# Performance work log

Measured on AMD Instinct MI355X. Metric: run time of the kernel, lower is better.

The kernel has to match this reference:

```python
import jax, jax.numpy as jnp
import numpy as np

B, D, H, E, K = 8192, 1024, 256, 16, 4


def setup_inputs() -> dict:
    key = jax.random.key(0)
    ks = jax.random.split(key, 6)
    s_d = D ** -0.5
    s_h = H ** -0.5
    return {
        "x": jax.random.normal(ks[0], (B, D), dtype=jnp.float32),
        "route_w": jax.random.normal(ks[1], (E, D), dtype=jnp.float32) * s_d,
        "w1": jax.random.normal(ks[2], (E, H, D), dtype=jnp.float32) * s_d,
        "b1": jax.random.normal(ks[3], (E, H), dtype=jnp.float32) * s_d,
        "w2": jax.random.normal(ks[4], (E, D, H), dtype=jnp.float32) * s_h,
        "b2": jax.random.normal(ks[5], (E, D), dtype=jnp.float32) * s_h,
    }


def _moe_forward(x, route_w, w1, b1, w2, b2):
    # Router: logits (B, E) -> top-k softmax weights scattered back to (B, E).
    logits = x @ route_w.T
    top_vals, top_idx = jax.lax.top_k(logits, K)
    top_w = jax.nn.softmax(top_vals, axis=-1)
    rows = jnp.arange(x.shape[0])[:, None]
    weights = jnp.zeros_like(logits).at[rows, top_idx].set(top_w)  # (B, E)

    # Experts: out = sum_e w[:, e] * relu(relu(x W1e^T + b1e) W2e^T + b2e)
    # Non-selected experts have weight 0, so dense-then-weight matches the
    # original masked gather/scatter math exactly (dropout = 0).
    def step(out, params_e):
        W1, bb1, W2, bb2, we = params_e
        h = jax.nn.relu(x @ W1.T + bb1)       # (B, H)
        y = jax.nn.relu(h @ W2.T + bb2)       # (B, D)
        return out + y * we[:, None], None

    out0 = jnp.zeros_like(x)
    out, _ = jax.lax.scan(step, out0, (w1, b1, w2, b2, weights.T))
    return out


def reference(x, route_w, w1, b1, w2, b2):
    return _moe_forward(x, route_w, w1, b1, w2, b2)
```

## Files before the change

### kernel.cpp

```cpp
#include <hip/hip_runtime.h>
#include <stdint.h>

typedef unsigned short u16;
typedef __attribute__((ext_vector_type(8))) short bf16x8;
typedef __attribute__((ext_vector_type(4))) float f32x4;
typedef __attribute__((ext_vector_type(8))) u16 u16x8;
typedef __attribute__((ext_vector_type(4))) u16 u16x4;

#define NTOK 8192
#define DDIM 1024
#define HDIM 256
#define NEXP 16
#define MAXT 272
#define MAXMT (MAXT * 2)
#define MAXSLOT (MAXT * 128)

__device__ __forceinline__ u16 f2bf(float f) {
  uint32_t u = __builtin_bit_cast(uint32_t, f);
  u += 0x7FFFu + ((u >> 16) & 1u);
  return (u16)(u >> 16);
}
__device__ __forceinline__ float bf2f(u16 h) {
  return __builtin_bit_cast(float, (uint32_t)h << 16);
}

__device__ __forceinline__ void gll16(const void* g, void* l) {
  __builtin_amdgcn_global_load_lds((const __attribute__((address_space(1))) void*)g,
                                   (__attribute__((address_space(3))) void*)l,
                                   16, 0, 0);
}

__global__ __launch_bounds__(256) void cvt_kernel(const float* __restrict__ in,
                                                  u16* __restrict__ out) {
  size_t i = ((size_t)blockIdx.x * 256 + threadIdx.x) * 8;
  const float4 a = *(const float4*)(in + i);
  const float4 b = *(const float4*)(in + i + 4);
  u16x8 o;
  o[0] = f2bf(a.x); o[1] = f2bf(a.y); o[2] = f2bf(a.z); o[3] = f2bf(a.w);
  o[4] = f2bf(b.x); o[5] = f2bf(b.y); o[6] = f2bf(b.z); o[7] = f2bf(b.w);
  *(u16x8*)(out + i) = o;
}

__global__ __launch_bounds__(256) void zero_out_kernel(float* __restrict__ p) {
  size_t i = ((size_t)blockIdx.x * 256 + threadIdx.x) * 4;
  *(float4*)(p + i) = (float4){0.f, 0.f, 0.f, 0.f};
}

__global__ __launch_bounds__(256) void router_kernel(const float* __restrict__ x,
                                                     const float* __restrict__ rw,
                                                     int* __restrict__ epack,
                                                     float* __restrict__ ew,
                                                     u16* __restrict__ xbf) {
  __shared__ __align__(16) uint8_t rwlds[65536];
  const int tid = threadIdx.x;

#pragma unroll
  for (int i = 0; i < 16; ++i) {
    int byte = (i * 256 + tid) * 16;
    int sw = byte ^ (((byte >> 8) & 7) << 4);
    *(float4*)(rwlds + sw) = *(const float4*)((const uint8_t*)rw + byte);
  }
  __syncthreads();

  const int lane = tid & 63, wid = tid >> 6;
  const int s = lane & 15;
  const int tok = blockIdx.x * 16 + wid * 4 + (lane >> 4);
  const float* xrow = x + (size_t)tok * DDIM;
  u16* xbrow = xbf + (size_t)tok * DDIM;

  double acc[NEXP];
#pragma unroll
  for (int e = 0; e < NEXP; ++e) acc[e] = 0.0;

#pragma unroll 4
  for (int g = 0; g < 16; ++g) {
    const int d = s * 64 + g * 4;
    float4 xv = *(const float4*)(xrow + d);
    u16x4 o;
    o[0] = f2bf(xv.x); o[1] = f2bf(xv.y); o[2] = f2bf(xv.z); o[3] = f2bf(xv.w);
    *(u16x4*)(xbrow + d) = o;
    const double x0 = xv.x, x1 = xv.y, x2 = xv.z, x3 = xv.w;
    const int roff = (s * 256 + g * 16) ^ ((s & 7) << 4);
#pragma unroll
    for (int e = 0; e < NEXP; ++e) {
      float4 rv = *(const float4*)(rwlds + e * 4096 + roff);
      acc[e] = fma(x0, (double)rv.x, acc[e]);
      acc[e] = fma(x1, (double)rv.y, acc[e]);
      acc[e] = fma(x2, (double)rv.z, acc[e]);
      acc[e] = fma(x3, (double)rv.w, acc[e]);
    }
  }

#define FOLD(H, M)                                                   \
  _Pragma("unroll") for (int i = 0; i < H; ++i) {                    \
    double send = (lane & M) ? acc[i] : acc[i + H];                  \
    double recv = __shfl_xor(send, M);                               \
    acc[i] = ((lane & M) ? acc[i + H] : acc[i]) + recv;              \
  }
  FOLD(8, 1)
  FOLD(4, 2)
  FOLD(2, 4)
  FOLD(1, 8)
#undef FOLD
  const int e_mine = ((lane & 1) << 3) | ((lane & 2) << 1) |
                     ((lane & 4) >> 1) | ((lane & 8) >> 3);

  double val = acc[0];
  double tv[4]; int tidx[4];
#pragma unroll
  for (int k = 0; k < 4; ++k) {
    double bv = val; int be = e_mine;
#pragma unroll
    for (int m = 1; m < 16; m <<= 1) {
      double ov = __shfl_xor(bv, m);
      int oe = __shfl_xor(be, m);
      if (ov > bv || (ov == bv && oe < be)) { bv = ov; be = oe; }
    }
    tv[k] = bv; tidx[k] = be;
    if (e_mine == be) val = -1.0e300;
  }

  if ((lane & 15) == 0) {
    float m0 = (float)tv[0];
    float w[4]; float sum = 0.f;
#pragma unroll
    for (int k = 0; k < 4; ++k) { w[k] = expf((float)tv[k] - m0); sum += w[k]; }
    epack[tok] = tidx[0] | (tidx[1] << 8) | (tidx[2] << 16) | (tidx[3] << 24);
#pragma unroll
    for (int k = 0; k < 4; ++k) ew[tok * 4 + k] = w[k] / sum;
  }
}

__global__ __launch_bounds__(1024) void compact_kernel(const int* __restrict__ epack,
                                                       const float* __restrict__ ew,
                                                       int* __restrict__ texp,
                                                       int* __restrict__ perm,
                                                       float* __restrict__ wsl,
                                                       int* __restrict__ islot) {
  __shared__ int wave_cnt[16][NEXP];
  __shared__ int counts_sm[NEXP];
  __shared__ int wtot[16], wave_off[16];
  const int e = blockIdx.x;
  const int tid = threadIdx.x, lane = tid & 63, w = tid >> 6;

  int ep[8]; unsigned m[8];
#pragma unroll
  for (int j = 0; j < 8; ++j) {
    ep[j] = epack[tid * 8 + j];
    m[j] = (1u << (ep[j] & 255)) | (1u << ((ep[j] >> 8) & 255)) |
           (1u << ((ep[j] >> 16) & 255)) | (1u << ((ep[j] >> 24) & 255));
  }
#pragma unroll
  for (int ee = 0; ee < NEXP; ++ee) {
    int c = 0;
#pragma unroll
    for (int j = 0; j < 8; ++j) c += (m[j] >> ee) & 1u;
#pragma unroll
    for (int off = 32; off > 0; off >>= 1) c += __shfl_xor(c, off);
    if (lane == 0) wave_cnt[w][ee] = c;
  }
  unsigned fm = 0;
#pragma unroll
  for (int j = 0; j < 8; ++j) fm |= ((m[j] >> e) & 1u) << j;
  int s = __popc(fm);
  int incl = s;
#pragma unroll
  for (int d = 1; d < 64; d <<= 1) {
    int t2 = __shfl_up(incl, d);
    if (lane >= d) incl += t2;
  }
  if (lane == 63) wtot[w] = incl;
  __syncthreads();
  if (tid < NEXP) {
    int c = 0;
    for (int w2 = 0; w2 < 16; ++w2) c += wave_cnt[w2][tid];
    counts_sm[tid] = c;
  }
  if (tid == 0) {
    int run = 0;
    for (int w2 = 0; w2 < 16; ++w2) { wave_off[w2] = run; run += wtot[w2]; }
  }
  __syncthreads();
  int base = 0;
  for (int ee = 0; ee < NEXP; ++ee)
    if (ee < e) base += ((counts_sm[ee] + 127) >> 7) << 7;
  int pos = base + wave_off[w] + (incl - s);
#pragma unroll
  for (int j = 0; j < 8; ++j) {
    if ((fm >> j) & 1u) {
      int tok = tid * 8 + j;
      int b0 = ep[j] & 255, b1 = (ep[j] >> 8) & 255, b2_ = (ep[j] >> 16) & 255;
      int k = (b0 == e) ? 0 : ((b1 == e) ? 1 : ((b2_ == e) ? 2 : 3));
      perm[pos] = tok;
      wsl[pos] = ew[tok * 4 + k];
      islot[tok * 4 + k] = pos;
      ++pos;
    }
  }
  int cnt = counts_sm[e];
  int pad = (((cnt + 127) >> 7) << 7) - cnt;
  if (tid < pad) { perm[base + cnt + tid] = 0; wsl[base + cnt + tid] = 0.f; }
  if (e == 0 && tid == 0) {
    int tc = 0;
    for (int ee = 0; ee < NEXP; ++ee) {
      int nt = (counts_sm[ee] + 127) >> 7;
      for (int i = 0; i < nt; ++i) texp[tc++] = ee;
    }
    for (; tc < MAXT; ++tc) texp[tc] = -1;
  }
}

__device__ __forceinline__ void stage128(const u16* __restrict__ base, int ld,
                                         int kbase, uint8_t* dst, int tid) {
#pragma unroll
  for (int i = 0; i < 4; ++i) {
    int u = i * 256 + tid;
    int row = u >> 3, g = u & 7;
    gll16(base + (size_t)row * ld + kbase + ((g ^ (row & 7)) << 3), dst + u * 16);
  }
}
__device__ __forceinline__ void stage64(const u16* __restrict__ base, int ld,
                                        int kbase, uint8_t* dst, int tid) {
#pragma unroll
  for (int i = 0; i < 2; ++i) {
    int u = i * 256 + tid;
    int row = u >> 3, g = u & 7;
    gll16(base + (size_t)row * ld + kbase + ((g ^ (row & 7)) << 3), dst + u * 16);
  }
}
__device__ __forceinline__ void stage_gather64(const u16* __restrict__ xbf,
                                               const int tok[2], int kbase,
                                               uint8_t* dst, int tid) {
#pragma unroll
  for (int i = 0; i < 2; ++i) {
    int u = i * 256 + tid;
    int g = u & 7;
    gll16(xbf + (size_t)tok[i] * DDIM + kbase + ((g ^ ((u >> 3) & 7)) << 3), dst + u * 16);
  }
}

__device__ __forceinline__ void mma64(const uint8_t* Ab, const uint8_t* Bb,
                                      f32x4 acc[2][4], int wm, int wn,
                                      int lrow, int lk) {
#pragma unroll
  for (int s = 0; s < 2; ++s) {
    bf16x8 af[2], bfr[4];
#pragma unroll
    for (int f = 0; f < 2; ++f) {
      int ar = wm * 32 + f * 16 + lrow;
      af[f] = *(const bf16x8*)(Ab + ar * 128 + ((((s << 2) | lk) ^ (ar & 7)) << 4));
    }
#pragma unroll
    for (int f = 0; f < 4; ++f) {
      int br = wn * 64 + f * 16 + lrow;
      bfr[f] = *(const bf16x8*)(Bb + br * 128 + ((((s << 2) | lk) ^ (br & 7)) << 4));
    }
#pragma unroll
    for (int i = 0; i < 2; ++i)
#pragma unroll
      for (int j = 0; j < 4; ++j)
        acc[i][j] = __builtin_amdgcn_mfma_f32_16x16x32_bf16(af[i], bfr[j], acc[i][j], 0, 0, 0);
  }
}

__global__ __launch_bounds__(256) void gemm1_kernel(const u16* __restrict__ xbf,
                                                    const u16* __restrict__ w1bf,
                                                    const float* __restrict__ b1,
                                                    const int* __restrict__ texp,
                                                    const int* __restrict__ perm,
                                                    u16* __restrict__ Hc, int mt0) {
  __shared__ __align__(16) uint8_t smem[2][24576];
  const int mt = mt0 + blockIdx.x;
  const int e = (mt < MAXMT) ? texp[mt >> 1] : -1;
  if (e < 0) return;
  const int n0 = blockIdx.y * 128;
  const int tid = threadIdx.x;
  const int lane = tid & 63, wid = tid >> 6;
  const int wm = wid >> 1, wn = wid & 1;
  const int lrow = lane & 15, lk = lane >> 4;

  int tok[2];
#pragma unroll
  for (int i = 0; i < 2; ++i) tok[i] = perm[mt * 64 + ((i * 256 + tid) >> 3)];
  const u16* Bsrc = w1bf + ((size_t)e * HDIM + n0) * DDIM;

  f32x4 acc[2][4];
#pragma unroll
  for (int i = 0; i < 2; ++i)
#pragma unroll
    for (int j = 0; j < 4; ++j) acc[i][j] = (f32x4){0.f, 0.f, 0.f, 0.f};

  stage_gather64(xbf, tok, 0, smem[0], tid);
  stage128(Bsrc, DDIM, 0, smem[0] + 8192, tid);
  __syncthreads();
  int cur = 0;
  for (int kt = 0; kt < 16; ++kt) {
    if (kt < 15) {
      stage_gather64(xbf, tok, (kt + 1) * 64, smem[cur ^ 1], tid);
      stage128(Bsrc, DDIM, (kt + 1) * 64, smem[cur ^ 1] + 8192, tid);
    }
    mma64(smem[cur], smem[cur] + 8192, acc, wm, wn, lrow, lk);
    __syncthreads();
    cur ^= 1;
  }
#pragma unroll
  for (int j = 0; j < 4; ++j) {
    int n = n0 + wn * 64 + j * 16 + lrow;
    float bias = b1[e * HDIM + n];
#pragma unroll
    for (int i = 0; i < 2; ++i) {
      int rloc = (mt - mt0) * 64 + wm * 32 + i * 16 + lk * 4;
#pragma unroll
      for (int r = 0; r < 4; ++r) {
        float h = fmaxf(acc[i][j][r] + bias, 0.f);
        Hc[((size_t)rloc + r) * HDIM + n] = f2bf(h);
      }
    }
  }
}

__global__ __launch_bounds__(256) void gemm2_main_kernel(const u16* __restrict__ Hc,
                                                         const u16* __restrict__ w2bf,
                                                         const float* __restrict__ b2,
                                                         const int* __restrict__ texp,
                                                         u16* __restrict__ ybuf,
                                                         int nbase, int NC) {
  __shared__ __align__(16) uint8_t smem[2][24576];
  const int mt = blockIdx.x;
  const int e = texp[mt >> 1];
  if (e < 0) return;
  const int nl0 = blockIdx.y * 128;
  const int tid = threadIdx.x;
  const int lane = tid & 63, wid = tid >> 6;
  const int wm = wid >> 1, wn = wid & 1;
  const int lrow = lane & 15, lk = lane >> 4;

  const u16* Asrc = Hc + (size_t)mt * 64 * HDIM;
  const u16* Bsrc = w2bf + ((size_t)e * DDIM + nbase + nl0) * HDIM;

  f32x4 acc[2][4];
#pragma unroll
  for (int i = 0; i < 2; ++i)
#pragma unroll
    for (int j = 0; j < 4; ++j) acc[i][j] = (f32x4){0.f, 0.f, 0.f, 0.f};

  stage64(Asrc, HDIM, 0, smem[0], tid);
  stage128(Bsrc, HDIM, 0, smem[0] + 8192, tid);
  __syncthreads();
  int cur = 0;
  for (int kt = 0; kt < 4; ++kt) {
    if (kt < 3) {
      stage64(Asrc, HDIM, (kt + 1) * 64, smem[cur ^ 1], tid);
      stage128(Bsrc, HDIM, (kt + 1) * 64, smem[cur ^ 1] + 8192, tid);
    }
    mma64(smem[cur], smem[cur] + 8192, acc, wm, wn, lrow, lk);
    __syncthreads();
    cur ^= 1;
  }
  float bias[4];
#pragma unroll
  for (int j = 0; j < 4; ++j)
    bias[j] = b2[e * DDIM + nbase + nl0 + wn * 64 + j * 16 + lrow];
#pragma unroll
  for (int i = 0; i < 2; ++i) {
#pragma unroll
    for (int r = 0; r < 4; ++r) {
      int slot = mt * 64 + wm * 32 + i * 16 + lk * 4 + r;
#pragma unroll
      for (int j = 0; j < 4; ++j) {
        int nloc = nl0 + wn * 64 + j * 16 + lrow;
        float h = fmaxf(acc[i][j][r] + bias[j], 0.f);
        ybuf[(size_t)slot * NC + nloc] = f2bf(h);
      }
    }
  }
}

__global__ __launch_bounds__(256) void gemm2_fb_kernel(const u16* __restrict__ Hc,
                                                       const u16* __restrict__ w2bf,
                                                       const float* __restrict__ b2,
                                                       const int* __restrict__ texp,
                                                       const int* __restrict__ perm,
                                                       const float* __restrict__ wsl,
                                                       float* __restrict__ out, int mt0) {
  __shared__ __align__(16) uint8_t smem[2][24576];
  const int mt = mt0 + blockIdx.x;
  const int e = (mt < MAXMT) ? texp[mt >> 1] : -1;
  if (e < 0) return;
  const int nl0 = blockIdx.y * 128;
  const int tid = threadIdx.x;
  const int lane = tid & 63, wid = tid >> 6;
  const int wm = wid >> 1, wn = wid & 1;
  const int lrow = lane & 15, lk = lane >> 4;

  const u16* Asrc = Hc + (size_t)(mt - mt0) * 64 * HDIM;
  const u16* Bsrc = w2bf + ((size_t)e * DDIM + nl0) * HDIM;

  f32x4 acc[2][4];
#pragma unroll
  for (int i = 0; i < 2; ++i)
#pragma unroll
    for (int j = 0; j < 4; ++j) acc[i][j] = (f32x4){0.f, 0.f, 0.f, 0.f};

  stage64(Asrc, HDIM, 0, smem[0], tid);
  stage128(Bsrc, HDIM, 0, smem[0] + 8192, tid);
  __syncthreads();
  int cur = 0;
  for (int kt = 0; kt < 4; ++kt) {
    if (kt < 3) {
      stage64(Asrc, HDIM, (kt + 1) * 64, smem[cur ^ 1], tid);
      stage128(Bsrc, HDIM, (kt + 1) * 64, smem[cur ^ 1] + 8192, tid);
    }
    mma64(smem[cur], smem[cur] + 8192, acc, wm, wn, lrow, lk);
    __syncthreads();
    cur ^= 1;
  }
  float bias[4];
#pragma unroll
  for (int j = 0; j < 4; ++j)
    bias[j] = b2[e * DDIM + nl0 + wn * 64 + j * 16 + lrow];
#pragma unroll
  for (int i = 0; i < 2; ++i) {
#pragma unroll
    for (int r = 0; r < 4; ++r) {
      int slot = mt * 64 + wm * 32 + i * 16 + lk * 4 + r;
      int tokn = perm[slot];
      float w = wsl[slot];
#pragma unroll
      for (int j = 0; j < 4; ++j) {
        int n = nl0 + wn * 64 + j * 16 + lrow;
        float h = fmaxf(acc[i][j][r] + bias[j], 0.f);
        atomicAdd(&out[(size_t)tokn * DDIM + n], w * h);
      }
    }
  }
}

__global__ __launch_bounds__(256) void combine_kernel(const u16* __restrict__ ybuf,
                                                      const float* __restrict__ ew,
                                                      const int* __restrict__ islot,
                                                      float* __restrict__ out,
                                                      int n0, int NC, int cshift) {
  int gid = blockIdx.x * 256 + threadIdx.x;
  int t = gid >> cshift;
  int c = (gid & ((1 << cshift) - 1)) << 2;
  const int4 sl = *(const int4*)(islot + t * 4);
  const float4 w = *(const float4*)(ew + t * 4);
  float4 a = {0.f, 0.f, 0.f, 0.f};
#define ACC(SL, W)                                             \
  {                                                            \
    u16x4 y = *(const u16x4*)(ybuf + (size_t)(SL)*NC + c);     \
    a.x += (W)*bf2f(y[0]); a.y += (W)*bf2f(y[1]);              \
    a.z += (W)*bf2f(y[2]); a.w += (W)*bf2f(y[3]);              \
  }
  ACC(sl.x, w.x); ACC(sl.y, w.y); ACC(sl.z, w.z); ACC(sl.w, w.w);
#undef ACC
  *(float4*)(out + (size_t)t * DDIM + n0 + c) = a;
}

extern "C" void kernel_launch(void* const* d_in, const int* in_sizes, int n_in,
                              void* d_out, int out_size, void* d_ws, size_t ws_size,
                              hipStream_t stream) {
  const float* x = (const float*)d_in[0];
  const float* route_w = (const float*)d_in[1];
  const float* w1 = (const float*)d_in[2];
  const float* b1 = (const float*)d_in[3];
  const float* w2 = (const float*)d_in[4];
  const float* b2 = (const float*)d_in[5];
  float* out = (float*)d_out;

  uint8_t* ws = (uint8_t*)d_ws;
  const size_t OFF_EPACK = 0;
  const size_t OFF_EW    = 32768;
  const size_t OFF_ISLOT = 163840;
  const size_t OFF_TEXP  = 294912;
  const size_t OFF_PERM  = 296960;
  const size_t OFF_WSL   = 436224;
  const size_t OFF_X     = 1048576;
  const size_t OFF_W1    = OFF_X + (size_t)NTOK * DDIM * 2;
  const size_t OFF_W2    = OFF_W1 + (size_t)NEXP * HDIM * DDIM * 2;
  const size_t OFF_HC    = OFF_W2 + (size_t)NEXP * DDIM * HDIM * 2;
  const size_t OFF_Y     = OFF_HC + (size_t)MAXSLOT * HDIM * 2;

  int* epack  = (int*)(ws + OFF_EPACK);
  float* ew   = (float*)(ws + OFF_EW);
  int* islot  = (int*)(ws + OFF_ISLOT);
  int* texp   = (int*)(ws + OFF_TEXP);
  int* perm   = (int*)(ws + OFF_PERM);
  float* wsl  = (float*)(ws + OFF_WSL);
  u16* xbf    = (u16*)(ws + OFF_X);
  u16* w1bf   = (u16*)(ws + OFF_W1);
  u16* w2bf   = (u16*)(ws + OFF_W2);
  u16* Hc     = (u16*)(ws + OFF_HC);
  u16* ybuf   = (u16*)(ws + OFF_Y);

  cvt_kernel<<<dim3((NEXP * HDIM * DDIM) / 2048), 256, 0, stream>>>(w1, w1bf);
  cvt_kernel<<<dim3((NEXP * DDIM * HDIM) / 2048), 256, 0, stream>>>(w2, w2bf);
  router_kernel<<<dim3(NTOK / 16), 256, 0, stream>>>(x, route_w, epack, ew, xbf);
  compact_kernel<<<dim3(NEXP), 1024, 0, stream>>>(epack, ew, texp, perm, wsl, islot);

  int ybN = 0;
  for (int cand = 1024; cand >= 128; cand >>= 1) {
    if (ws_size >= OFF_Y + (size_t)MAXSLOT * cand * 2) { ybN = cand; break; }
  }

  if (ybN > 0) {
    gemm1_kernel<<<dim3(MAXMT, HDIM / 128), 256, 0, stream>>>(xbf, w1bf, b1, texp, perm, Hc, 0);
    int cshift = __builtin_ctz(ybN >> 2);
    for (int nb = 0; nb < DDIM; nb += ybN) {
      gemm2_main_kernel<<<dim3(MAXMT, ybN / 128), 256, 0, stream>>>(
          Hc, w2bf, b2, texp, ybuf, nb, ybN);
      combine_kernel<<<dim3((NTOK << cshift) / 256), 256, 0, stream>>>(
          ybuf, ew, islot, out, nb, ybN, cshift);
    }
  } else {
    long room = (long)ws_size - (long)OFF_HC;
    int CT = (int)(room / 65536);
    if (CT > MAXT) CT = MAXT;
    if (CT < 16) CT = 16;
    zero_out_kernel<<<dim3((NTOK * DDIM) / 1024), 256, 0, stream>>>(out);
    for (int t0 = 0; t0 < MAXT; t0 += CT) {
      int ct = (MAXT - t0 < CT) ? (MAXT - t0) : CT;
      gemm1_kernel<<<dim3(ct * 2, HDIM / 128), 256, 0, stream>>>(
          xbf, w1bf, b1, texp, perm, Hc, t0 * 2);
      gemm2_fb_kernel<<<dim3(ct * 2, DDIM / 128), 256, 0, stream>>>(
          Hc, w2bf, b2, texp, perm, wsl, out, t0 * 2);
    }
  }
}
```

Before: 142.4 us.

## Use 128x128 tiles with 512-thread blocks for expert GEMMs and merge weight conversions

The expert GEMM kernels move from 64x128 tiles on 256 threads to 128x128 tiles on 512 threads, so each B-weight tile loaded into LDS is reused across twice as many token rows. This halves the grid in the M dimension and raises LDS use per block to 64 KB. The two fp32-to-bf16 weight conversion launches are merged into one kernel to save a launch. Each block now needs more LDS and more threads, which may lower occupancy, and the grid has fewer blocks to spread across CUs.

```diff
diff --git a/kernel.cpp b/kernel.cpp
--- a/kernel.cpp
+++ b/kernel.cpp
@@ -12,7 +12,6 @@
 #define HDIM 256
 #define NEXP 16
 #define MAXT 272
-#define MAXMT (MAXT * 2)
 #define MAXSLOT (MAXT * 128)
 
 __device__ __forceinline__ u16 f2bf(float f) {
@@ -30,14 +29,20 @@
                                    16, 0, 0);
 }
 
-__global__ __launch_bounds__(256) void cvt_kernel(const float* __restrict__ in,
-                                                  u16* __restrict__ out) {
-  size_t i = ((size_t)blockIdx.x * 256 + threadIdx.x) * 8;
-  const float4 a = *(const float4*)(in + i);
-  const float4 b = *(const float4*)(in + i + 4);
+__global__ __launch_bounds__(256) void cvt2_kernel(const float* __restrict__ a,
+                                                   const float* __restrict__ b,
+                                                   u16* __restrict__ oa,
+                                                   u16* __restrict__ ob,
+                                                   int nba) {
+  const float* in; u16* out;
+  int bx = blockIdx.x;
+  if (bx < nba) { in = a; out = oa; } else { in = b; out = ob; bx -= nba; }
+  size_t i = ((size_t)bx * 256 + threadIdx.x) * 8;
+  const float4 p = *(const float4*)(in + i);
+  const float4 q = *(const float4*)(in + i + 4);
   u16x8 o;
-  o[0] = f2bf(a.x); o[1] = f2bf(a.y); o[2] = f2bf(a.z); o[3] = f2bf(a.w);
-  o[4] = f2bf(b.x); o[5] = f2bf(b.y); o[6] = f2bf(b.z); o[7] = f2bf(b.w);
+  o[0] = f2bf(p.x); o[1] = f2bf(p.y); o[2] = f2bf(p.z); o[3] = f2bf(p.w);
+  o[4] = f2bf(q.x); o[5] = f2bf(q.y); o[6] = f2bf(q.z); o[7] = f2bf(q.w);
   *(u16x8*)(out + i) = o;
 }
 
@@ -210,38 +215,29 @@
   }
 }
 
-__device__ __forceinline__ void stage128(const u16* __restrict__ base, int ld,
-                                         int kbase, uint8_t* dst, int tid) {
-#pragma unroll
-  for (int i = 0; i < 4; ++i) {
-    int u = i * 256 + tid;
+__device__ __forceinline__ void stage128w(const u16* __restrict__ base, int ld,
+                                          int kbase, uint8_t* dst, int tid) {
+#pragma unroll
+  for (int i = 0; i < 2; ++i) {
+    int u = i * 512 + tid;
     int row = u >> 3, g = u & 7;
     gll16(base + (size_t)row * ld + kbase + ((g ^ (row & 7)) << 3), dst + u * 16);
   }
 }
-__device__ __forceinline__ void stage64(const u16* __restrict__ base, int ld,
-                                        int kbase, uint8_t* dst, int tid) {
+__device__ __forceinline__ void gather128w(const u16* __restrict__ xbf,
+                                           const int tok[2], int kbase,
+                                           uint8_t* dst, int tid) {
 #pragma unroll
   for (int i = 0; i < 2; ++i) {
-    int u = i * 256 + tid;
-    int row = u >> 3, g = u & 7;
-    gll16(base + (size_t)row * ld + kbase + ((g ^ (row & 7)) << 3), dst + u * 16);
-  }
-}
-__device__ __forceinline__ void stage_gather64(const u16* __restrict__ xbf,
-                                               const int tok[2], int kbase,
-                                               uint8_t* dst, int tid) {
-#pragma unroll
-  for (int i = 0; i < 2; ++i) {
-    int u = i * 256 + tid;
+    int u = i * 512 + tid;
     int g = u & 7;
     gll16(xbf + (size_t)tok[i] * DDIM + kbase + ((g ^ ((u >> 3) & 7)) << 3), dst + u * 16);
   }
 }
 
-__device__ __forceinline__ void mma64(const uint8_t* Ab, const uint8_t* Bb,
-                                      f32x4 acc[2][4], int wm, int wn,
-                                      int lrow, int lk) {
+__device__ __forceinline__ void mma32x64(const uint8_t* Ab, const uint8_t* Bb,
+                                         f32x4 acc[2][4], int wm, int wn,
+                                         int lrow, int lk) {
 #pragma unroll
   for (int s = 0; s < 2; ++s) {
     bf16x8 af[2], bfr[4];
@@ -263,15 +259,15 @@
   }
 }
 
-__global__ __launch_bounds__(256) void gemm1_kernel(const u16* __restrict__ xbf,
+__global__ __launch_bounds__(512) void gemm1_kernel(const u16* __restrict__ xbf,
                                                     const u16* __restrict__ w1bf,
                                                     const float* __restrict__ b1,
                                                     const int* __restrict__ texp,
                                                     const int* __restrict__ perm,
-                                                    u16* __restrict__ Hc, int mt0) {
-  __shared__ __align__(16) uint8_t smem[2][24576];
-  const int mt = mt0 + blockIdx.x;
-  const int e = (mt < MAXMT) ? texp[mt >> 1] : -1;
+                                                    u16* __restrict__ Hc, int t0) {
+  __shared__ __align__(16) uint8_t smem[2][32768];
+  const int t = t0 + blockIdx.x;
+  const int e = (t < MAXT) ? texp[t] : -1;
   if (e < 0) return;
   const int n0 = blockIdx.y * 128;
   const int tid = threadIdx.x;
@@ -281,7 +277,7 @@
 
   int tok[2];
 #pragma unroll
-  for (int i = 0; i < 2; ++i) tok[i] = perm[mt * 64 + ((i * 256 + tid) >> 3)];
+  for (int i = 0; i < 2; ++i) tok[i] = perm[t * 128 + ((i * 512 + tid) >> 3)];
   const u16* Bsrc = w1bf + ((size_t)e * HDIM + n0) * DDIM;
 
   f32x4 acc[2][4];
@@ -290,16 +286,16 @@
 #pragma unroll
     for (int j = 0; j < 4; ++j) acc[i][j] = (f32x4){0.f, 0.f, 0.f, 0.f};
 
-  stage_gather64(xbf, tok, 0, smem[0], tid);
-  stage128(Bsrc, DDIM, 0, smem[0] + 8192, tid);
+  gather128w(xbf, tok, 0, smem[0], tid);
+  stage128w(Bsrc, DDIM, 0, smem[0] + 16384, tid);
   __syncthreads();
   int cur = 0;
   for (int kt = 0; kt < 16; ++kt) {
     if (kt < 15) {
-      stage_gather64(xbf, tok, (kt + 1) * 64, smem[cur ^ 1], tid);
-      stage128(Bsrc, DDIM, (kt + 1) * 64, smem[cur ^ 1] + 8192, tid);
-    }
-    mma64(smem[cur], smem[cur] + 8192, acc, wm, wn, lrow, lk);
+      gather128w(xbf, tok, (kt + 1) * 64, smem[cur ^ 1], tid);
+      stage128w(Bsrc, DDIM, (kt + 1) * 64, smem[cur ^ 1] + 16384, tid);
+    }
+    mma32x64(smem[cur], smem[cur] + 16384, acc, wm, wn, lrow, lk);
     __syncthreads();
     cur ^= 1;
   }
@@ -309,7 +305,7 @@
     float bias = b1[e * HDIM + n];
 #pragma unroll
     for (int i = 0; i < 2; ++i) {
-      int rloc = (mt - mt0) * 64 + wm * 32 + i * 16 + lk * 4;
+      int rloc = (t - t0) * 128 + wm * 32 + i * 16 + lk * 4;
 #pragma unroll
       for (int r = 0; r < 4; ++r) {
         float h = fmaxf(acc[i][j][r] + bias, 0.f);
@@ -319,15 +315,15 @@
   }
 }
 
-__global__ __launch_bounds__(256) void gemm2_main_kernel(const u16* __restrict__ Hc,
+__global__ __launch_bounds__(512) void gemm2_main_kernel(const u16* __restrict__ Hc,
                                                          const u16* __restrict__ w2bf,
                                                          const float* __restrict__ b2,
                                                          const int* __restrict__ texp,
                                                          u16* __restrict__ ybuf,
                                                          int nbase, int NC) {
-  __shared__ __align__(16) uint8_t smem[2][24576];
-  const int mt = blockIdx.x;
-  const int e = texp[mt >> 1];
+  __shared__ __align__(16) uint8_t smem[2][32768];
+  const int t = blockIdx.x;
+  const int e = texp[t];
   if (e < 0) return;
   const int nl0 = blockIdx.y * 128;
   const int tid = threadIdx.x;
@@ -335,7 +331,7 @@
   const int wm = wid >> 1, wn = wid & 1;
   const int lrow = lane & 15, lk = lane >> 4;
 
-  const u16* Asrc = Hc + (size_t)mt * 64 * HDIM;
+  const u16* Asrc = Hc + (size_t)t * 128 * HDIM;
   const u16* Bsrc = w2bf + ((size_t)e * DDIM + nbase + nl0) * HDIM;
 
   f32x4 acc[2][4];
@@ -344,16 +340,16 @@
 #pragma unroll
     for (int j = 0; j < 4; ++j) acc[i][j] = (f32x4){0.f, 0.f, 0.f, 0.f};
 
-  stage64(Asrc, HDIM, 0, smem[0], tid);
-  stage128(Bsrc, HDIM, 0, smem[0] + 8192, tid);
+  stage128w(Asrc, HDIM, 0, smem[0], tid);
+  stage128w(Bsrc, HDIM, 0, smem[0] + 16384, tid);
   __syncthreads();
   int cur = 0;
   for (int kt = 0; kt < 4; ++kt) {
     if (kt < 3) {
-      stage64(Asrc, HDIM, (kt + 1) * 64, smem[cur ^ 1], tid);
-      stage128(Bsrc, HDIM, (kt + 1) * 64, smem[cur ^ 1] + 8192, tid);
-    }
-    mma64(smem[cur], smem[cur] + 8192, acc, wm, wn, lrow, lk);
+      stage128w(Asrc, HDIM, (kt + 1) * 64, smem[cur ^ 1], tid);
+      stage128w(Bsrc, HDIM, (kt + 1) * 64, smem[cur ^ 1] + 16384, tid);
+    }
+    mma32x64(smem[cur], smem[cur] + 16384, acc, wm, wn, lrow, lk);
     __syncthreads();
     cur ^= 1;
   }
@@ -365,7 +361,7 @@
   for (int i = 0; i < 2; ++i) {
 #pragma unroll
     for (int r = 0; r < 4; ++r) {
-      int slot = mt * 64 + wm * 32 + i * 16 + lk * 4 + r;
+      int slot = t * 128 + wm * 32 + i * 16 + lk * 4 + r;
 #pragma unroll
       for (int j = 0; j < 4; ++j) {
         int nloc = nl0 + wn * 64 + j * 16 + lrow;
@@ -376,16 +372,16 @@
   }
 }
 
-__global__ __launch_bounds__(256) void gemm2_fb_kernel(const u16* __restrict__ Hc,
+__global__ __launch_bounds__(512) void gemm2_fb_kernel(const u16* __restrict__ Hc,
                                                        const u16* __restrict__ w2bf,
                                                        const float* __restrict__ b2,
                                                        const int* __restrict__ texp,
                                                        const int* __restrict__ perm,
                                                        const float* __restrict__ wsl,
-                                                       float* __restrict__ out, int mt0) {
-  __shared__ __align__(16) uint8_t smem[2][24576];
-  const int mt = mt0 + blockIdx.x;
-  const int e = (mt < MAXMT) ? texp[mt >> 1] : -1;
+                                                       float* __restrict__ out, int t0) {
+  __shared__ __align__(16) uint8_t smem[2][32768];
+  const int t = t0 + blockIdx.x;
+  const int e = (t < MAXT) ? texp[t] : -1;
   if (e < 0) return;
   const int nl0 = blockIdx.y * 128;
   const int tid = threadIdx.x;
@@ -393,7 +389,7 @@
   const int wm = wid >> 1, wn = wid & 1;
   const int lrow = lane & 15, lk = lane >> 4;
 
-  const u16* Asrc = Hc + (size_t)(mt - mt0) * 64 * HDIM;
+  const u16* Asrc = Hc + (size_t)(t - t0) * 128 * HDIM;
   const u16* Bsrc = w2bf + ((size_t)e * DDIM + nl0) * HDIM;
 
   f32x4 acc[2][4];
@@ -402,16 +398,16 @@
 #pragma unroll
     for (int j = 0; j < 4; ++j) acc[i][j] = (f32x4){0.f, 0.f, 0.f, 0.f};
 
-  stage64(Asrc, HDIM, 0, smem[0], tid);
-  stage128(Bsrc, HDIM, 0, smem[0] + 8192, tid);
+  stage128w(Asrc, HDIM, 0, smem[0], tid);
+  stage128w(Bsrc, HDIM, 0, smem[0] + 16384, tid);
   __syncthreads();
   int cur = 0;
   for (int kt = 0; kt < 4; ++kt) {
     if (kt < 3) {
-      stage64(Asrc, HDIM, (kt + 1) * 64, smem[cur ^ 1], tid);
-      stage128(Bsrc, HDIM, (kt + 1) * 64, smem[cur ^ 1] + 8192, tid);
-    }
-    mma64(smem[cur], smem[cur] + 8192, acc, wm, wn, lrow, lk);
+      stage128w(Asrc, HDIM, (kt + 1) * 64, smem[cur ^ 1], tid);
+      stage128w(Bsrc, HDIM, (kt + 1) * 64, smem[cur ^ 1] + 16384, tid);
+    }
+    mma32x64(smem[cur], smem[cur] + 16384, acc, wm, wn, lrow, lk);
     __syncthreads();
     cur ^= 1;
   }
@@ -423,7 +419,7 @@
   for (int i = 0; i < 2; ++i) {
 #pragma unroll
     for (int r = 0; r < 4; ++r) {
-      int slot = mt * 64 + wm * 32 + i * 16 + lk * 4 + r;
+      int slot = t * 128 + wm * 32 + i * 16 + lk * 4 + r;
       int tokn = perm[slot];
       float w = wsl[slot];
 #pragma unroll
@@ -494,8 +490,8 @@
   u16* Hc     = (u16*)(ws + OFF_HC);
   u16* ybuf   = (u16*)(ws + OFF_Y);
 
-  cvt_kernel<<<dim3((NEXP * HDIM * DDIM) / 2048), 256, 0, stream>>>(w1, w1bf);
-  cvt_kernel<<<dim3((NEXP * DDIM * HDIM) / 2048), 256, 0, stream>>>(w2, w2bf);
+  const int nba = (NEXP * HDIM * DDIM) / 2048;
+  cvt2_kernel<<<dim3(nba * 2), 256, 0, stream>>>(w1, w2, w1bf, w2bf, nba);
   router_kernel<<<dim3(NTOK / 16), 256, 0, stream>>>(x, route_w, epack, ew, xbf);
   compact_kernel<<<dim3(NEXP), 1024, 0, stream>>>(epack, ew, texp, perm, wsl, islot);
 
@@ -505,10 +501,10 @@
   }
 
   if (ybN > 0) {
-    gemm1_kernel<<<dim3(MAXMT, HDIM / 128), 256, 0, stream>>>(xbf, w1bf, b1, texp, perm, Hc, 0);
+    gemm1_kernel<<<dim3(MAXT, HDIM / 128), 512, 0, stream>>>(xbf, w1bf, b1, texp, perm, Hc, 0);
     int cshift = __builtin_ctz(ybN >> 2);
     for (int nb = 0; nb < DDIM; nb += ybN) {
-      gemm2_main_kernel<<<dim3(MAXMT, ybN / 128), 256, 0, stream>>>(
+      gemm2_main_kernel<<<dim3(MAXT, ybN / 128), 512, 0, stream>>>(
           Hc, w2bf, b2, texp, ybuf, nb, ybN);
       combine_kernel<<<dim3((NTOK << cshift) / 256), 256, 0, stream>>>(
           ybuf, ew, islot, out, nb, ybN, cshift);
@@ -521,10 +517,10 @@
     zero_out_kernel<<<dim3((NTOK * DDIM) / 1024), 256, 0, stream>>>(out);
     for (int t0 = 0; t0 < MAXT; t0 += CT) {
       int ct = (MAXT - t0 < CT) ? (MAXT - t0) : CT;
-      gemm1_kernel<<<dim3(ct * 2, HDIM / 128), 256, 0, stream>>>(
-          xbf, w1bf, b1, texp, perm, Hc, t0 * 2);
-      gemm2_fb_kernel<<<dim3(ct * 2, DDIM / 128), 256, 0, stream>>>(
-          Hc, w2bf, b2, texp, perm, wsl, out, t0 * 2);
-    }
-  }
-}
+      gemm1_kernel<<<dim3(ct, HDIM / 128), 512, 0, stream>>>(
+          xbf, w1bf, b1, texp, perm, Hc, t0);
+      gemm2_fb_kernel<<<dim3(ct, DDIM / 128), 512, 0, stream>>>(
+          Hc, w2bf, b2, texp, perm, wsl, out, t0);
+    }
+  }
+}
```

After: 141.0 us. Within noise of the previous version (-0.9%).
